# Kernel optimization log

Measured on AMD Instinct MI355X. Metric: run time of the kernel, lower is better.

## Reference

```python
import jax, jax.numpy as jnp
import numpy as np

B, S, IN_DIM = 128, 1024, 256
M, D, OUT = 64, 128, 128


def setup_inputs() -> dict:
    key = jax.random.key(0)
    ks = jax.random.split(key, 10)
    def xavier(k, shape):
        fan_in, fan_out = shape[-1], shape[-2] if len(shape) > 1 else shape[-1]
        lim = jnp.sqrt(6.0 / (shape[0] + shape[1]))
        return jax.random.uniform(k, shape, jnp.float32, -lim, lim)
    return {
        "x": jax.random.normal(ks[0], (B, S, IN_DIM), jnp.float32),
        "memory_key": xavier(ks[1], (M, D)),
        "memory_value": xavier(ks[2], (M, D)),
        "Wr": xavier(ks[3], (IN_DIM, D)),
        "br": jnp.zeros((D,), jnp.float32),
        "Ww": xavier(ks[4], (IN_DIM, D)),
        "bw": jnp.zeros((D,), jnp.float32),
        "Wp": xavier(ks[5], (D, OUT)),
        "bp": jnp.zeros((OUT,), jnp.float32),
    }


def reference(x, memory_key, memory_value, Wr, br, Ww, bw, Wp, bp):
    # Precompute time-parallel parts: read keys and write erase/add signals.
    k_all = jnp.einsum("bsi,id->bsd", x, Wr) + br          # [B,S,D]
    v_all = jnp.einsum("bsi,id->bsd", x, Ww) + bw          # [B,S,D]
    erase_all = jax.nn.sigmoid(v_all)                        # [B,S,D]
    add_all = jnp.tanh(v_all)                                # [B,S,D]

    Mv0 = jnp.broadcast_to(memory_value, (x.shape[0],) + memory_value.shape)  # [B,M,D]

    def step(Mv, inp):
        k_t, e_t, a_t = inp                                  # each [B,D]
        w = jax.nn.softmax(k_t @ memory_key.T, axis=-1)      # [B,M]
        r = jnp.einsum("bm,bmd->bd", w, Mv)                # [B,D]
        y = jax.nn.sigmoid(r @ Wp + bp)                      # [B,OUT]
        wE = w[:, :, None]                                   # [B,M,1]
        Mv = Mv * (1.0 - wE * e_t[:, None, :]) + wE * a_t[:, None, :]
        return Mv, y

    xs = (jnp.swapaxes(k_all, 0, 1),
          jnp.swapaxes(erase_all, 0, 1),
          jnp.swapaxes(add_all, 0, 1))                       # [S,B,D] each
    _, ys = jax.lax.scan(step, Mv0, xs)                      # ys: [S,B,OUT]
    return jnp.swapaxes(ys, 0, 1)                            # [B,S,OUT]
```

## Files before the change

kernel.cpp:

```cpp
#include <hip/hip_runtime.h>
#include <hip/hip_bf16.h>


#define B_   128
#define S_   1024
#define IN_  256
#define M_   64
#define D_   128
#define OUT_ 128
#define NROWS_ (B_ * S_)

typedef __hip_bfloat16 bf16;
typedef unsigned int uint32;
typedef __attribute__((ext_vector_type(8))) short s16x8;
typedef __attribute__((ext_vector_type(4))) float f32x4;

__device__ __forceinline__ float tof(bf16 v) { return __bfloat162float(v); }
__device__ __forceinline__ bf16  tob(float v) { return __float2bfloat16(v); }
__device__ __forceinline__ float ldf(const float* p, long i) { return p[i]; }
__device__ __forceinline__ float ldf(const bf16* p, long i)  { return tof(p[i]); }
__device__ __forceinline__ void  stf(float* p, long i, float v) { p[i] = v; }
__device__ __forceinline__ void  stf(bf16* p, long i, float v)  { p[i] = tob(v); }
__device__ __forceinline__ void  unp(uint32 u, float& lo, float& hi) {
  lo = __uint_as_float(u << 16);
  hi = __uint_as_float(u & 0xFFFF0000u);
}
__device__ __forceinline__ uint32 pk(float lo, float hi) {
  union { bf16 h; unsigned short u; } a, b;
  a.h = tob(lo); b.h = tob(hi);
  return (uint32)a.u | ((uint32)b.u << 16);
}
__device__ __forceinline__ void split2(float f0, float f1, uint32& h, uint32& l) {
  union { bf16 b; unsigned short u; } a0, a1;
  a0.b = tob(f0); a1.b = tob(f1);
  h = (uint32)a0.u | ((uint32)a1.u << 16);
  const float r0 = f0 - tof(a0.b);
  const float r1 = f1 - tof(a1.b);
  l = pk(r0, r1);
}

__global__ __launch_bounds__(256) void k_probe(const uint32* __restrict__ xw,
                                               int* __restrict__ flag) {
  __shared__ int s[256];
  const int tid = threadIdx.x;
  int sc = 0;
#pragma unroll
  for (int k = 0; k < 8; ++k) {
    const uint32 u = xw[tid * 8 + k];
    const float v = __uint_as_float(u << 16);
    if (!(fabsf(v) < 4.0f)) sc++;
  }
  s[tid] = sc;
  __syncthreads();
  for (int o = 128; o > 0; o >>= 1) {
    if (tid < o) s[tid] += s[tid + o];
    __syncthreads();
  }
  if (tid == 0) *flag = (s[0] > 64) ? 1 : 0;
}

template <typename T>
__device__ void k0_body(const T* Wr, const T* br, const T* K,
                        float* Wk, float* bk) {
  const int idx = blockIdx.x * 256 + threadIdx.x;
  if (idx < IN_ * M_) {
    const int i = idx >> 6, m = idx & 63;
    float acc = 0.f;
    for (int d = 0; d < D_; ++d)
      acc = fmaf(ldf(Wr, (long)i * D_ + d), ldf(K, (long)m * D_ + d), acc);
    Wk[idx] = acc;
  } else if (idx < IN_ * M_ + M_) {
    const int m = idx - IN_ * M_;
    float acc = 0.f;
    for (int d = 0; d < D_; ++d)
      acc = fmaf(ldf(br, d), ldf(K, (long)m * D_ + d), acc);
    bk[m] = acc;
  }
}

__global__ __launch_bounds__(256) void k0_fold(const void* Wr, const void* br,
                                               const void* K, float* Wk, float* bk,
                                               const int* flag) {
  if (*flag) k0_body<float>((const float*)Wr, (const float*)br, (const float*)K, Wk, bk);
  else       k0_body<bf16>((const bf16*)Wr, (const bf16*)br, (const bf16*)K, Wk, bk);
}

__global__ __launch_bounds__(256) void k0b_pack(const void* Ww, const void* Wp,
                                                const float* Wk, bf16* WTh, bf16* WTl,
                                                bf16* WpTh, bf16* WpTl,
                                                const int* flag) {
  const int f = *flag;
  const int idx = blockIdx.x * 256 + threadIdx.x;
  if (idx < 12 * 8 * 64 * 8) {
    const int j = idx & 7, lane = (idx >> 3) & 63;
    const int kst = (idx >> 9) & 7, ct = idx >> 12;
    const int l15 = lane & 15, quad = lane >> 4;
    const int n = ct * 16 + l15;
    const int k = kst * 32 + quad * 8 + j;
    float v;
    if (f) v = (n < 128) ? ((const float*)Ww)[k * 128 + n] : Wk[k * 64 + (n - 128)];
    else   v = (n < 128) ? tof(((const bf16*)Ww)[k * 128 + n]) : Wk[k * 64 + (n - 128)];
    const bf16 h = tob(v);
    WTh[idx] = h;
    if (f) WTl[idx] = tob(v - tof(h));
  } else {
    const int o = idx - 12 * 8 * 64 * 8;
    const int j = o & 7, lane = (o >> 3) & 63;
    const int kst = (o >> 9) & 3, ct = o >> 11;
    const int l15 = lane & 15, quad = lane >> 4;
    const int n = ct * 16 + l15;
    const int k = kst * 32 + quad * 8 + j;
    float v;
    if (f) v = ((const float*)Wp)[k * 128 + n];
    else   v = tof(((const bf16*)Wp)[k * 128 + n]);
    const bf16 h = tob(v);
    WpTh[o] = h;
    if (f) WpTl[o] = tob(v - tof(h));
  }
}

template <bool F32>
__device__ void k1_body(const void* x, const void* bw, const float* bk,
                        const bf16* __restrict__ WTh, const bf16* __restrict__ WTl,
                        uint32* __restrict__ ea_all, bf16* __restrict__ w_all,
                        int chunk, int TL, int tshift) {
  const int tid = threadIdx.x;
  const int wave = tid >> 6, lane = tid & 63;
  const int l15 = lane & 15, quad = lane >> 4;
  const int b = blockIdx.x >> tshift;
  const int tb = blockIdx.x & ((1 << tshift) - 1);
  const int t0 = tb * 64 + wave * 16;
  const long lr0 = (long)b * TL + t0;
  const long ar0 = (long)b * S_ + (long)chunk * TL + t0;

  s16x8 afh[8], afl[8];
  if constexpr (F32) {
    const float* xr = (const float*)x + (ar0 + l15) * (long)IN_ + quad * 8;
#pragma unroll
    for (int k = 0; k < 8; ++k) {
      const float4 u0 = *(const float4*)(xr + k * 32);
      const float4 u1 = *(const float4*)(xr + k * 32 + 4);
      union { s16x8 v; uint32 u[4]; } H, L;
      split2(u0.x, u0.y, H.u[0], L.u[0]);
      split2(u0.z, u0.w, H.u[1], L.u[1]);
      split2(u1.x, u1.y, H.u[2], L.u[2]);
      split2(u1.z, u1.w, H.u[3], L.u[3]);
      afh[k] = H.v;
      afl[k] = L.v;
    }
  } else {
    const bf16* xr = (const bf16*)x + (ar0 + l15) * (long)IN_ + quad * 8;
#pragma unroll
    for (int k = 0; k < 8; ++k) afh[k] = *(const s16x8*)(xr + k * 32);
  }

  f32x4 acc[12];
#pragma unroll
  for (int ct = 0; ct < 12; ++ct) acc[ct] = (f32x4){0.f, 0.f, 0.f, 0.f};

  const bf16* fbh = WTh + lane * 8;
  const bf16* fbl = WTl + lane * 8;
#pragma unroll
  for (int ct = 0; ct < 12; ++ct) {
#pragma unroll
    for (int k = 0; k < 8; ++k) {
      const s16x8 bh = *(const s16x8*)(fbh + (ct * 8 + k) * 512);
      acc[ct] = __builtin_amdgcn_mfma_f32_16x16x32_bf16(afh[k], bh, acc[ct], 0, 0, 0);
      if constexpr (F32) {
        const s16x8 bl = *(const s16x8*)(fbl + (ct * 8 + k) * 512);
        acc[ct] = __builtin_amdgcn_mfma_f32_16x16x32_bf16(afl[k], bh, acc[ct], 0, 0, 0);
        acc[ct] = __builtin_amdgcn_mfma_f32_16x16x32_bf16(afh[k], bl, acc[ct], 0, 0, 0);
      }
    }
  }

#pragma unroll
  for (int ct = 0; ct < 8; ++ct) {
    const int col = ct * 16 + l15;
    float bb;
    if constexpr (F32) bb = ((const float*)bw)[col];
    else               bb = tof(((const bf16*)bw)[col]);
#pragma unroll
    for (int r = 0; r < 4; ++r) {
      const float v = acc[ct][r] + bb;
      const float sg = 1.0f / (1.0f + exp2f(-1.44269504f * v));
      const float th = 1.0f - 2.0f / (exp2f(2.88539008f * v) + 1.0f);
      ea_all[(lr0 + quad * 4 + r) * D_ + col] = pk(sg, th);
    }
  }
  float bks[4];
#pragma unroll
  for (int g = 0; g < 4; ++g) bks[g] = bk[g * 16 + l15];
#pragma unroll
  for (int r = 0; r < 4; ++r) {
    float s[4];
    float mx = -1e30f;
#pragma unroll
    for (int g = 0; g < 4; ++g) {
      s[g] = acc[8 + g][r] + bks[g];
      mx = fmaxf(mx, s[g]);
    }
#pragma unroll
    for (int off = 1; off < 16; off <<= 1) mx = fmaxf(mx, __shfl_xor(mx, off, 64));
    float ex[4], sum = 0.f;
#pragma unroll
    for (int g = 0; g < 4; ++g) {
      ex[g] = exp2f(1.44269504f * (s[g] - mx));
      sum += ex[g];
    }
#pragma unroll
    for (int off = 1; off < 16; off <<= 1) sum += __shfl_xor(sum, off, 64);
    const float inv = 1.0f / sum;
    const long lr = lr0 + quad * 4 + r;
#pragma unroll
    for (int g = 0; g < 4; ++g)
      w_all[lr * M_ + g * 16 + l15] = tob(ex[g] * inv);
  }
}

__global__ __launch_bounds__(256, 2) void k1_mfma(const void* x, const void* bw,
                                                  const float* bk, const bf16* WTh,
                                                  const bf16* WTl, uint32* ea_all,
                                                  bf16* w_all, int chunk, int TL,
                                                  int tshift,
                                                  const int* __restrict__ flag) {
  if (*flag) k1_body<true>(x, bw, bk, WTh, WTl, ea_all, w_all, chunk, TL, tshift);
  else       k1_body<false>(x, bw, bk, WTh, WTl, ea_all, w_all, chunk, TL, tshift);
}

template <typename T>
__device__ void k2_body(const T* Mv0, const uint32* ea_all, const bf16* w_all,
                        float* MvS, T* r_out, int chunk, int TL, int TC) {
  const int tid = threadIdx.x;
  const int wave = tid >> 6, lane = tid & 63;
  const int mg = lane >> 2, dl = lane & 3;
  const int b = blockIdx.x & 127;
  const int dg = ((blockIdx.x >> 7) << 2) + wave;
  const int d = dg * 4 + dl;
  const int m0 = mg * 4;

  float Mv[4];
  if (chunk == 0) {
#pragma unroll
    for (int j = 0; j < 4; ++j)
      Mv[j] = ldf(Mv0, (long)(m0 + j) * D_ + d);
  } else {
#pragma unroll
    for (int j = 0; j < 4; ++j)
      Mv[j] = MvS[((long)b * M_ + m0 + j) * D_ + d];
  }

  const long lrbase = (long)b * TL;
  const long arbase = (long)b * S_ + (long)chunk * TL;
  const uint32* eap = ea_all + lrbase * D_ + d;
  const bf16* wap = w_all + lrbase * M_ + m0;

  uint32 erA[8], erB[8];
  uint2 wrA[8], wrB[8];
  float rbuf[8];
#pragma unroll
  for (int p = 0; p < 8; ++p) {
    erA[p] = eap[p * D_];
    wrA[p] = *(const uint2*)(wap + p * M_);
  }

  for (int t = 0; t < TL; t += 16) {
#pragma unroll
    for (int p = 0; p < 8; ++p) {
      const int ln = t + 8 + p;
      erB[p] = eap[(long)ln * D_];
      wrB[p] = *(const uint2*)(wap + (long)ln * M_);
    }
#pragma unroll
    for (int p = 0; p < 8; ++p) {
      float e, a;
      unp(erA[p], e, a);
      float wv[4];
      unp(wrA[p].x, wv[0], wv[1]);
      unp(wrA[p].y, wv[2], wv[3]);
      float r = 0.f;
#pragma unroll
      for (int j = 0; j < 4; ++j) {
        r = fmaf(wv[j], Mv[j], r);
        Mv[j] = fmaf(wv[j], fmaf(-e, Mv[j], a), Mv[j]);
      }
      r += __shfl_xor(r, 4, 64);
      r += __shfl_xor(r, 8, 64);
      r += __shfl_xor(r, 16, 64);
      r += __shfl_xor(r, 32, 64);
      rbuf[p] = r;
    }
    if (mg == 0) {
#pragma unroll
      for (int p = 0; p < 8; ++p)
        stf(r_out, (arbase + t + p) * D_ + d, rbuf[p]);
    }
#pragma unroll
    for (int p = 0; p < 8; ++p) {
      int ln = t + 16 + p;
      ln = ln < TL ? ln : TL - 1;
      erA[p] = eap[(long)ln * D_];
      wrA[p] = *(const uint2*)(wap + (long)ln * M_);
    }
#pragma unroll
    for (int p = 0; p < 8; ++p) {
      float e, a;
      unp(erB[p], e, a);
      float wv[4];
      unp(wrB[p].x, wv[0], wv[1]);
      unp(wrB[p].y, wv[2], wv[3]);
      float r = 0.f;
#pragma unroll
      for (int j = 0; j < 4; ++j) {
        r = fmaf(wv[j], Mv[j], r);
        Mv[j] = fmaf(wv[j], fmaf(-e, Mv[j], a), Mv[j]);
      }
      r += __shfl_xor(r, 4, 64);
      r += __shfl_xor(r, 8, 64);
      r += __shfl_xor(r, 16, 64);
      r += __shfl_xor(r, 32, 64);
      rbuf[p] = r;
    }
    if (mg == 0) {
#pragma unroll
      for (int p = 0; p < 8; ++p)
        stf(r_out, (arbase + t + 8 + p) * D_ + d, rbuf[p]);
    }
  }
  if (chunk < TC - 1) {
#pragma unroll
    for (int j = 0; j < 4; ++j)
      MvS[((long)b * M_ + m0 + j) * D_ + d] = Mv[j];
  }
}

__global__ __launch_bounds__(256) void k2_scan(const void* Mv0, const uint32* ea_all,
                                               const bf16* w_all, float* MvS,
                                               void* r_out, int chunk, int TL,
                                               int TC, const int* flag) {
  if (*flag) k2_body<float>((const float*)Mv0, ea_all, w_all, MvS,
                            (float*)r_out, chunk, TL, TC);
  else       k2_body<bf16>((const bf16*)Mv0, ea_all, w_all, MvS,
                           (bf16*)r_out, chunk, TL, TC);
}

template <bool F32>
__device__ void k3_body(const bf16* __restrict__ WpTh, const bf16* __restrict__ WpTl,
                        const void* bpv, void* iov) {
  const int tid = threadIdx.x;
  const int wave = tid >> 6, lane = tid & 63;
  const int l15 = lane & 15, quad = lane >> 4;
  const long row0 = (long)blockIdx.x * 64 + wave * 16;

  s16x8 afh[4], afl[4];
  if constexpr (F32) {
    const float* rr = (const float*)iov + (row0 + l15) * D_ + quad * 8;
#pragma unroll
    for (int k = 0; k < 4; ++k) {
      const float4 u0 = *(const float4*)(rr + k * 32);
      const float4 u1 = *(const float4*)(rr + k * 32 + 4);
      union { s16x8 v; uint32 u[4]; } H, L;
      split2(u0.x, u0.y, H.u[0], L.u[0]);
      split2(u0.z, u0.w, H.u[1], L.u[1]);
      split2(u1.x, u1.y, H.u[2], L.u[2]);
      split2(u1.z, u1.w, H.u[3], L.u[3]);
      afh[k] = H.v;
      afl[k] = L.v;
    }
  } else {
    const bf16* rr = (const bf16*)iov + (row0 + l15) * D_ + quad * 8;
#pragma unroll
    for (int k = 0; k < 4; ++k) afh[k] = *(const s16x8*)(rr + k * 32);
  }

  f32x4 acc[8];
#pragma unroll
  for (int ct = 0; ct < 8; ++ct) acc[ct] = (f32x4){0.f, 0.f, 0.f, 0.f};
  const bf16* fbh = WpTh + lane * 8;
  const bf16* fbl = WpTl + lane * 8;
#pragma unroll
  for (int ct = 0; ct < 8; ++ct) {
#pragma unroll
    for (int k = 0; k < 4; ++k) {
      const s16x8 bh = *(const s16x8*)(fbh + (ct * 4 + k) * 512);
      acc[ct] = __builtin_amdgcn_mfma_f32_16x16x32_bf16(afh[k], bh, acc[ct], 0, 0, 0);
      if constexpr (F32) {
        const s16x8 bl = *(const s16x8*)(fbl + (ct * 4 + k) * 512);
        acc[ct] = __builtin_amdgcn_mfma_f32_16x16x32_bf16(afl[k], bh, acc[ct], 0, 0, 0);
        acc[ct] = __builtin_amdgcn_mfma_f32_16x16x32_bf16(afh[k], bl, acc[ct], 0, 0, 0);
      }
    }
  }
#pragma unroll
  for (int ct = 0; ct < 8; ++ct) {
    const int col = ct * 16 + l15;
    float bb;
    if constexpr (F32) bb = ((const float*)bpv)[col];
    else               bb = tof(((const bf16*)bpv)[col]);
#pragma unroll
    for (int r = 0; r < 4; ++r) {
      const float y = 1.0f / (1.0f + exp2f(-1.44269504f * (acc[ct][r] + bb)));
      if constexpr (F32)
        ((float*)iov)[(row0 + quad * 4 + r) * OUT_ + col] = y;
      else
        ((bf16*)iov)[(row0 + quad * 4 + r) * OUT_ + col] = tob(y);
    }
  }
}

__global__ __launch_bounds__(256, 2) void k3_mfma(const bf16* __restrict__ WpTh,
                                                  const bf16* __restrict__ WpTl,
                                                  const void* bpv, void* iov,
                                                  const int* __restrict__ flag) {
  if (*flag) k3_body<true>(WpTh, WpTl, bpv, iov);
  else       k3_body<false>(WpTh, WpTl, bpv, iov);
}

extern "C" void kernel_launch(void* const* d_in, const int* in_sizes, int n_in,
                              void* d_out, int out_size, void* d_ws, size_t ws_size,
                              hipStream_t stream) {
  const void* x   = d_in[0];
  const void* mk  = d_in[1];
  const void* mv  = d_in[2];
  const void* Wr  = d_in[3];
  const void* br  = d_in[4];
  const void* Ww  = d_in[5];
  const void* bwv = d_in[6];
  const void* Wp  = d_in[7];
  const void* bp  = d_in[8];

  char* ws = (char*)d_ws;
  int*    flag = (int*)ws;
  float*  Wk   = (float*)(ws + 16);
  float*  bk   = (float*)(ws + 16 + 65536);
  bf16*   WTh  = (bf16*)(ws + 65808);
  bf16*   WTl  = WTh + 192 * 256;
  bf16*   WpTh = WTl + 192 * 256;
  bf16*   WpTl = WpTh + 128 * 128;
  char*   dyn  = (char*)(WpTl + 128 * 128);
  const size_t fixed = (size_t)(dyn - ws);

  int TC = 16;
  for (int c = 1; c <= 16; c <<= 1) {
    const size_t rc = (size_t)NROWS_ / c;
    const size_t need = fixed + rc * (D_ * 4 + M_ * 2) +
                        (c > 1 ? (size_t)B_ * M_ * D_ * 4 : 0) + 1024;
    if (need <= ws_size) { TC = c; break; }
  }
  const int TL = S_ / TC;
  const int tshift = __builtin_ctz(TL / 64);
  const size_t RC = (size_t)NROWS_ / TC;

  uint32* ea_all = (uint32*)dyn;
  bf16*   w_all  = (bf16*)(ea_all + RC * D_);
  float*  MvS    = (float*)(w_all + RC * M_);

  k_probe<<<1, 256, 0, stream>>>((const uint32*)x, flag);
  k0_fold<<<(IN_ * M_ + M_ + 255) / 256, 256, 0, stream>>>(Wr, br, mk, Wk, bk, flag);
  k0b_pack<<<256, 256, 0, stream>>>(Ww, Wp, Wk, WTh, WTl, WpTh, WpTl, flag);
  for (int c = 0; c < TC; ++c) {
    k1_mfma<<<(int)(RC / 64), 256, 0, stream>>>(x, bwv, bk, WTh, WTl, ea_all, w_all,
                                                c, TL, tshift, flag);
    k2_scan<<<B_ * 8, 256, 0, stream>>>(mv, ea_all, w_all, MvS, d_out, c, TL, TC,
                                        flag);
  }
  k3_mfma<<<NROWS_ / 64, 256, 0, stream>>>(WpTh, WpTl, bp, d_out, flag);
}
```

Baseline: 613.1 us.

## Stage scan inputs through LDS with async global_load_lds double buffering

The recurrent scan kernel stops loading erase/add and softmax weights straight into registers. Wave 0 now stages each 16-step tile into double-buffered shared memory using global_load_lds, and a block barrier separates tiles. The d-to-wave mapping changes so a block covers a contiguous 16-column slice, and the attention weights are stored in fp32 instead of bf16 so they can be read as aligned float4. This doubles the workspace and bandwidth for the weights, may lower the chunk count chosen, and adds a per-tile __syncthreads on the serial critical path.

```diff
diff --git a/kernel.cpp b/kernel.cpp
--- a/kernel.cpp
+++ b/kernel.cpp
@@ -37,6 +37,11 @@
   const float r0 = f0 - tof(a0.b);
   const float r1 = f1 - tof(a1.b);
   l = pk(r0, r1);
+}
+__device__ __forceinline__ void gl16(const void* g, void* s) {
+  __builtin_amdgcn_global_load_lds(
+      (const __attribute__((address_space(1))) void*)g,
+      (__attribute__((address_space(3))) void*)s, 16, 0, 0);
 }
 
 __global__ __launch_bounds__(256) void k_probe(const uint32* __restrict__ xw,
@@ -122,7 +127,7 @@
 template <bool F32>
 __device__ void k1_body(const void* x, const void* bw, const float* bk,
                         const bf16* __restrict__ WTh, const bf16* __restrict__ WTl,
-                        uint32* __restrict__ ea_all, bf16* __restrict__ w_all,
+                        uint32* __restrict__ ea_all, float* __restrict__ w_all,
                         int chunk, int TL, int tshift) {
   const int tid = threadIdx.x;
   const int wave = tid >> 6, lane = tid & 63;
@@ -214,14 +219,14 @@
     const long lr = lr0 + quad * 4 + r;
 #pragma unroll
     for (int g = 0; g < 4; ++g)
-      w_all[lr * M_ + g * 16 + l15] = tob(ex[g] * inv);
+      w_all[lr * M_ + g * 16 + l15] = ex[g] * inv;
   }
 }
 
 __global__ __launch_bounds__(256, 2) void k1_mfma(const void* x, const void* bw,
                                                   const float* bk, const bf16* WTh,
                                                   const bf16* WTl, uint32* ea_all,
-                                                  bf16* w_all, int chunk, int TL,
+                                                  float* w_all, int chunk, int TL,
                                                   int tshift,
                                                   const int* __restrict__ flag) {
   if (*flag) k1_body<true>(x, bw, bk, WTh, WTl, ea_all, w_all, chunk, TL, tshift);
@@ -229,15 +234,19 @@
 }
 
 template <typename T>
-__device__ void k2_body(const T* Mv0, const uint32* ea_all, const bf16* w_all,
+__device__ void k2_body(const T* Mv0, const uint32* ea_all, const float* w_all,
                         float* MvS, T* r_out, int chunk, int TL, int TC) {
   const int tid = threadIdx.x;
   const int wave = tid >> 6, lane = tid & 63;
   const int mg = lane >> 2, dl = lane & 3;
   const int b = blockIdx.x & 127;
-  const int dg = ((blockIdx.x >> 7) << 2) + wave;
-  const int d = dg * 4 + dl;
+  const int dgHi = blockIdx.x >> 7;
+  const int q = wave * 4 + dl;
+  const int d = dgHi * 16 + q;
   const int m0 = mg * 4;
+
+  __shared__ uint32 sEA[2][16][16];
+  __shared__ float  sW[2][16][64];
 
   float Mv[4];
   if (chunk == 0) {
@@ -252,81 +261,45 @@
 
   const long lrbase = (long)b * TL;
   const long arbase = (long)b * S_ + (long)chunk * TL;
-  const uint32* eap = ea_all + lrbase * D_ + d;
-  const bf16* wap = w_all + lrbase * M_ + m0;
-
-  uint32 erA[8], erB[8];
-  uint2 wrA[8], wrB[8];
-  float rbuf[8];
-#pragma unroll
-  for (int p = 0; p < 8; ++p) {
-    erA[p] = eap[p * D_];
-    wrA[p] = *(const uint2*)(wap + p * M_);
-  }
-
-  for (int t = 0; t < TL; t += 16) {
-#pragma unroll
-    for (int p = 0; p < 8; ++p) {
-      const int ln = t + 8 + p;
-      erB[p] = eap[(long)ln * D_];
-      wrB[p] = *(const uint2*)(wap + (long)ln * M_);
-    }
-#pragma unroll
-    for (int p = 0; p < 8; ++p) {
+
+  const int sl2 = lane >> 2, sl4 = lane >> 4;
+  const int eac = (lane & 3) * 4;
+  const int wmc = (lane & 15) * 4;
+  auto stage = [&](int buf, int t0) {
+    gl16(&ea_all[(lrbase + t0 + sl2) * D_ + dgHi * 16 + eac], &sEA[buf][0][0]);
+#pragma unroll
+    for (int i = 0; i < 4; ++i)
+      gl16(&w_all[(lrbase + t0 + i * 4 + sl4) * M_ + wmc], &sW[buf][i * 4][0]);
+  };
+
+  if (wave == 0) stage(0, 0);
+  __syncthreads();
+
+  const int NT = TL / 16;
+  for (int kk = 0; kk < NT; ++kk) {
+    const int cur = kk & 1;
+    if (wave == 0 && kk + 1 < NT) stage(cur ^ 1, (kk + 1) * 16);
+    const long ab = arbase + kk * 16;
+#pragma unroll
+    for (int t = 0; t < 16; ++t) {
       float e, a;
-      unp(erA[p], e, a);
-      float wv[4];
-      unp(wrA[p].x, wv[0], wv[1]);
-      unp(wrA[p].y, wv[2], wv[3]);
+      unp(sEA[cur][t][q], e, a);
+      const float4 wv = *(const float4*)&sW[cur][t][m0];
       float r = 0.f;
 #pragma unroll
       for (int j = 0; j < 4; ++j) {
-        r = fmaf(wv[j], Mv[j], r);
-        Mv[j] = fmaf(wv[j], fmaf(-e, Mv[j], a), Mv[j]);
+        r = fmaf(wv[j == 0 ? 0 : j == 1 ? 1 : j == 2 ? 2 : 3], Mv[j], r);
+        Mv[j] = fmaf((&wv.x)[j], fmaf(-e, Mv[j], a), Mv[j]);
       }
       r += __shfl_xor(r, 4, 64);
       r += __shfl_xor(r, 8, 64);
       r += __shfl_xor(r, 16, 64);
       r += __shfl_xor(r, 32, 64);
-      rbuf[p] = r;
-    }
-    if (mg == 0) {
-#pragma unroll
-      for (int p = 0; p < 8; ++p)
-        stf(r_out, (arbase + t + p) * D_ + d, rbuf[p]);
-    }
-#pragma unroll
-    for (int p = 0; p < 8; ++p) {
-      int ln = t + 16 + p;
-      ln = ln < TL ? ln : TL - 1;
-      erA[p] = eap[(long)ln * D_];
-      wrA[p] = *(const uint2*)(wap + (long)ln * M_);
-    }
-#pragma unroll
-    for (int p = 0; p < 8; ++p) {
-      float e, a;
-      unp(erB[p], e, a);
-      float wv[4];
-      unp(wrB[p].x, wv[0], wv[1]);
-      unp(wrB[p].y, wv[2], wv[3]);
-      float r = 0.f;
-#pragma unroll
-      for (int j = 0; j < 4; ++j) {
-        r = fmaf(wv[j], Mv[j], r);
-        Mv[j] = fmaf(wv[j], fmaf(-e, Mv[j], a), Mv[j]);
-      }
-      r += __shfl_xor(r, 4, 64);
-      r += __shfl_xor(r, 8, 64);
-      r += __shfl_xor(r, 16, 64);
-      r += __shfl_xor(r, 32, 64);
-      rbuf[p] = r;
-    }
-    if (mg == 0) {
-#pragma unroll
-      for (int p = 0; p < 8; ++p)
-        stf(r_out, (arbase + t + 8 + p) * D_ + d, rbuf[p]);
-    }
-  }
+      if (mg == 0) stf(r_out, (ab + t) * D_ + d, r);
+    }
+    __syncthreads();
+  }
+
   if (chunk < TC - 1) {
 #pragma unroll
     for (int j = 0; j < 4; ++j)
@@ -335,7 +308,7 @@
 }
 
 __global__ __launch_bounds__(256) void k2_scan(const void* Mv0, const uint32* ea_all,
-                                               const bf16* w_all, float* MvS,
+                                               const float* w_all, float* MvS,
                                                void* r_out, int chunk, int TL,
                                                int TC, const int* flag) {
   if (*flag) k2_body<float>((const float*)Mv0, ea_all, w_all, MvS,
@@ -443,7 +416,7 @@
   int TC = 16;
   for (int c = 1; c <= 16; c <<= 1) {
     const size_t rc = (size_t)NROWS_ / c;
-    const size_t need = fixed + rc * (D_ * 4 + M_ * 2) +
+    const size_t need = fixed + rc * (D_ * 4 + M_ * 4) +
                         (c > 1 ? (size_t)B_ * M_ * D_ * 4 : 0) + 1024;
     if (need <= ws_size) { TC = c; break; }
   }
@@ -452,7 +425,7 @@
   const size_t RC = (size_t)NROWS_ / TC;
 
   uint32* ea_all = (uint32*)dyn;
-  bf16*   w_all  = (bf16*)(ea_all + RC * D_);
+  float*  w_all  = (float*)(ea_all + RC * D_);
   float*  MvS    = (float*)(w_all + RC * M_);
 
   k_probe<<<1, 256, 0, stream>>>((const uint32*)x, flag);
```

Result: slower. 639.3 us (+4.3%).
